# Kernel tuning notes

Hardware: AMD Instinct MI355X
Metric: run time of the kernel (lower is better)

## Reference

```python
import jax, jax.numpy as jnp
import numpy as np
import math

D_K = 64

def setup_inputs() -> dict:
    key = jax.random.key(0)
    kq, kk, kv, km = jax.random.split(key, 4)
    B, H, S, D = 2, 16, 2048, D_K
    Q = jax.random.normal(kq, (B, H, S, D), dtype=jnp.float32)
    K = jax.random.normal(kk, (B, H, S, D), dtype=jnp.float32)
    V = jax.random.normal(kv, (B, H, S, D), dtype=jnp.float32)
    attn_mask = jax.random.randint(km, (B, 1, S, S), 0, 2, dtype=jnp.int32)
    return {"Q": Q, "K": K, "V": V, "attn_mask": attn_mask}

def reference(Q, K, V, attn_mask):
    # scores: [B, H, S, S]
    scores = jnp.einsum('bhqd,bhkd->bhqk', Q, K) / math.sqrt(D_K)
    scores = jnp.where(attn_mask == 0, jnp.float32(-1e9), scores)
    attn = jax.nn.softmax(scores, axis=-1)
    context = jnp.einsum('bhqk,bhkd->bhqd', attn, V)
    return (context, attn)
```

## Files before the change

### kernel.cpp

```cpp
#include <hip/hip_runtime.h>
#include <math.h>

#define B_   2
#define H_   16
#define S_   2048
#define D_   64
#define QT   16
#define NQT  (S_/QT)
#define NBLK (B_*H_*NQT)

typedef __attribute__((ext_vector_type(8))) short  bf16x8;
typedef __attribute__((ext_vector_type(8))) unsigned short u16x8;
typedef __attribute__((ext_vector_type(4))) float  f32x4;

static __device__ __forceinline__ short f2bf(float f) {
    union { float f; unsigned u; } x; x.f = f;
    unsigned r = x.u + 0x7fffu + ((x.u >> 16) & 1u);
    return (short)(r >> 16);
}
static __device__ __forceinline__ unsigned pk_bf16(float lo, float hi) {
    unsigned r;
    asm("v_cvt_pk_bf16_f32 %0, %1, %2" : "=v"(r) : "v"(lo), "v"(hi));
    return r;
}

__global__ __launch_bounds__(256) void cvt_scale_kernel(const float* __restrict__ src,
                                                        unsigned short* __restrict__ dst,
                                                        float scale) {
    const size_t i = ((size_t)blockIdx.x * 256 + threadIdx.x) * 8;
    const float4 a = *(const float4*)(src + i);
    const float4 b = *(const float4*)(src + i + 4);
    u16x8 o;
    o[0]=f2bf(a.x*scale); o[1]=f2bf(a.y*scale); o[2]=f2bf(a.z*scale); o[3]=f2bf(a.w*scale);
    o[4]=f2bf(b.x*scale); o[5]=f2bf(b.y*scale); o[6]=f2bf(b.z*scale); o[7]=f2bf(b.w*scale);
    *(u16x8*)(dst + i) = o;
}

__global__ __launch_bounds__(256) void cvtVT_kernel(const float* __restrict__ V,
                                                    unsigned short* __restrict__ Vt) {
    const int l  = threadIdx.x & 63;
    const int w  = threadIdx.x >> 6;
    const int bh = blockIdx.x >> 6;
    const int kc = (blockIdx.x & 63) * 32 + w * 8;
    const float* vp = V + ((size_t)bh * S_ + kc) * D_ + l;
    u16x8 o;
    #pragma unroll
    for (int j = 0; j < 8; ++j) o[j] = f2bf(vp[(size_t)j * D_]);
    *(u16x8*)(Vt + ((size_t)bh * D_ + l) * S_ + kc) = o;
}

__global__ __launch_bounds__(256) void maskbits_kernel(const int* __restrict__ M,
                                                       unsigned long long* __restrict__ bits) {
    const int w = threadIdx.x >> 6, l = threadIdx.x & 63;
    const size_t wl0 = (size_t)(blockIdx.x * 4 + w) * 32;
    for (int it = 0; it < 32; ++it) {
        const int mk = M[(wl0 + it) * 64 + l];
        const unsigned long long bm = __ballot(mk != 0);
        if (l == 0) bits[wl0 + it] = bm;
    }
}

template<int PREP>
__global__ __launch_bounds__(256, 4)
void sdpa_2pass_kernel(const float* __restrict__ Qf, const float* __restrict__ Kf,
                       const float* __restrict__ Vf, const int* __restrict__ Mi,
                       const unsigned short* __restrict__ Qs,
                       const unsigned short* __restrict__ Kb,
                       const unsigned short* __restrict__ Vt,
                       const unsigned* __restrict__ bits,
                       float* __restrict__ ctx_out, float* __restrict__ attn_out) {
    __shared__ unsigned mb[QT][66];
    __shared__ float red[4][QT][2];
    __shared__ float ctxp[4][QT][68];

    const int t = threadIdx.x;
    const int w = t >> 6;
    const int l = t & 63;
    const int x = l & 15;
    const int g = l >> 4;

    const int orig = blockIdx.x;
    const int swz  = (orig & 7) * (NBLK / 8) + (orig >> 3);
    const int bh   = swz >> 7;
    const int qt   = swz & 127;
    const int b    = bh >> 4;
    const int q0   = qt * QT;

    if (PREP) {
        #pragma unroll
        for (int i = 0; i < 4; ++i) {
            const int flat = t * 4 + i;
            mb[flat >> 6][flat & 63] =
                bits[((size_t)b * S_ + q0 + (flat >> 6)) * 64 + (flat & 63)];
        }
    }

    bf16x8 bq0, bq1;
    if (PREP) {
        const unsigned short* qp = Qs + ((size_t)bh * S_ + q0 + x) * D_ + g * 8;
        bq0 = *(const bf16x8*)qp;
        bq1 = *(const bf16x8*)(qp + 32);
    } else {
        const float* qp = Qf + ((size_t)bh * S_ + q0 + x) * D_ + g * 8;
        #pragma unroll
        for (int j = 0; j < 8; ++j) bq0[j] = f2bf(0.125f * qp[j]);
        #pragma unroll
        for (int j = 0; j < 8; ++j) bq1[j] = f2bf(0.125f * qp[32 + j]);
    }
    if (PREP) __syncthreads();

    auto qk_tile = [&](int ktg, f32x4& c) {
        bf16x8 ak0, ak1;
        if (PREP) {
            const unsigned short* kp = Kb + ((size_t)bh * S_ + ktg * 16 + x) * D_ + g * 8;
            ak0 = *(const bf16x8*)kp;
            ak1 = *(const bf16x8*)(kp + 32);
        } else {
            const float* kp = Kf + ((size_t)bh * S_ + ktg * 16 + x) * D_ + g * 8;
            #pragma unroll
            for (int j = 0; j < 8; ++j) ak0[j] = f2bf(kp[j]);
            #pragma unroll
            for (int j = 0; j < 8; ++j) ak1[j] = f2bf(kp[32 + j]);
        }
        c[0]=0.f; c[1]=0.f; c[2]=0.f; c[3]=0.f;
        c = __builtin_amdgcn_mfma_f32_16x16x32_bf16(ak0, bq0, c, 0, 0, 0);
        c = __builtin_amdgcn_mfma_f32_16x16x32_bf16(ak1, bq1, c, 0, 0, 0);
        if (PREP) {
            const unsigned word = mb[x][ktg >> 1];
            const int base = 16 * (ktg & 1) + 4 * g;
            #pragma unroll
            for (int r = 0; r < 4; ++r)
                if (!((word >> (base + r)) & 1u)) c[r] = -1e9f;
        } else {
            const int* mp = Mi + ((size_t)b * S_ + q0 + x) * S_ + ktg * 16 + 4 * g;
            #pragma unroll
            for (int r = 0; r < 4; ++r)
                if (!mp[r]) c[r] = -1e9f;
        }
    };

    float m = -INFINITY, ssum = 0.f;
    for (int kt = 0; kt < 32; ++kt) {
        f32x4 c; qk_tile(32 * w + kt, c);
        const float tm = fmaxf(fmaxf(c[0], c[1]), fmaxf(c[2], c[3]));
        const float nm = fmaxf(m, tm);
        ssum = ssum * __expf(m - nm)
             + __expf(c[0] - nm) + __expf(c[1] - nm)
             + __expf(c[2] - nm) + __expf(c[3] - nm);
        m = nm;
    }
    #pragma unroll
    for (int off = 16; off <= 32; off <<= 1) {
        const float mo = __shfl_xor(m, off), so = __shfl_xor(ssum, off);
        const float nm = fmaxf(m, mo);
        ssum = ssum * __expf(m - nm) + so * __expf(mo - nm);
        m = nm;
    }
    if (l < 16) { red[w][l][0] = m; red[w][l][1] = ssum; }
    __syncthreads();
    float M = -INFINITY, S = 0.f;
    #pragma unroll
    for (int wv = 0; wv < 4; ++wv) {
        const float mo = red[wv][x][0], so = red[wv][x][1];
        const float nm = fmaxf(M, mo);
        S = S * __expf(M - nm) + so * __expf(mo - nm);
        M = nm;
    }
    const float il = 1.0f / S;

    f32x4 ctx[4];
    #pragma unroll
    for (int ds = 0; ds < 4; ++ds) { ctx[ds][0]=0.f; ctx[ds][1]=0.f; ctx[ds][2]=0.f; ctx[ds][3]=0.f; }

    const int laneA = x + 32 * (g & 1);
    const int laneB = laneA + 16;
    const int tsel  = g >> 1;

    for (int s = 0; s < 16; ++s) {
        unsigned W00, W01, W10, W11;
        #pragma unroll
        for (int u = 0; u < 2; ++u) {
            const int ktg = 32 * w + 2 * s + u;
            f32x4 c; qk_tile(ktg, c);
            const float p0 = __expf(c[0] - M) * il, p1 = __expf(c[1] - M) * il;
            const float p2 = __expf(c[2] - M) * il, p3 = __expf(c[3] - M) * il;
            float4 o; o.x = p0; o.y = p1; o.z = p2; o.w = p3;
            *(float4*)(attn_out + ((size_t)bh * S_ + q0 + x) * S_ + ktg * 16 + 4 * g) = o;
            const unsigned lo = pk_bf16(p0, p1), hi = pk_bf16(p2, p3);
            if (u == 0) { W00 = lo; W01 = hi; } else { W10 = lo; W11 = hi; }
        }
        const unsigned a00 = __shfl(W00, laneA), a10 = __shfl(W10, laneA);
        const unsigned a01 = __shfl(W01, laneA), a11 = __shfl(W11, laneA);
        const unsigned b00 = __shfl(W00, laneB), b10 = __shfl(W10, laneB);
        const unsigned b01 = __shfl(W01, laneB), b11 = __shfl(W11, laneB);
        union { unsigned u[4]; bf16x8 v; } pa;
        pa.u[0] = tsel ? a10 : a00;
        pa.u[1] = tsel ? a11 : a01;
        pa.u[2] = tsel ? b10 : b00;
        pa.u[3] = tsel ? b11 : b01;
        const int kb = 512 * w + 32 * s;
        #pragma unroll
        for (int ds = 0; ds < 4; ++ds) {
            bf16x8 vb;
            if (PREP) {
                vb = *(const bf16x8*)(Vt + ((size_t)bh * D_ + 16 * ds + x) * S_ + kb + 8 * g);
            } else {
                const float* vp = Vf + ((size_t)bh * S_ + kb + 8 * g) * D_ + 16 * ds + x;
                #pragma unroll
                for (int j = 0; j < 8; ++j) vb[j] = f2bf(vp[(size_t)j * D_]);
            }
            ctx[ds] = __builtin_amdgcn_mfma_f32_16x16x32_bf16(pa.v, vb, ctx[ds], 0, 0, 0);
        }
    }

    #pragma unroll
    for (int ds = 0; ds < 4; ++ds)
        #pragma unroll
        for (int r = 0; r < 4; ++r)
            ctxp[w][4 * g + r][16 * ds + x] = ctx[ds][r];
    __syncthreads();
    {
        const int base = t * 4;
        const int qr = base >> 6, c0 = base & 63;
        float4 o;
        o.x = ctxp[0][qr][c0+0] + ctxp[1][qr][c0+0] + ctxp[2][qr][c0+0] + ctxp[3][qr][c0+0];
        o.y = ctxp[0][qr][c0+1] + ctxp[1][qr][c0+1] + ctxp[2][qr][c0+1] + ctxp[3][qr][c0+1];
        o.z = ctxp[0][qr][c0+2] + ctxp[1][qr][c0+2] + ctxp[2][qr][c0+2] + ctxp[3][qr][c0+2];
        o.w = ctxp[0][qr][c0+3] + ctxp[1][qr][c0+3] + ctxp[2][qr][c0+3] + ctxp[3][qr][c0+3];
        *(float4*)(ctx_out + ((size_t)bh * S_ + q0 + qr) * D_ + c0) = o;
    }
}

extern "C" void kernel_launch(void* const* d_in, const int* in_sizes, int n_in,
                              void* d_out, int out_size, void* d_ws, size_t ws_size,
                              hipStream_t stream) {
    const float* Q = (const float*)d_in[0];
    const float* K = (const float*)d_in[1];
    const float* V = (const float*)d_in[2];
    const int*   M = (const int*)d_in[3];

    float* ctx  = (float*)d_out;
    float* attn = (float*)d_out + (size_t)B_ * H_ * S_ * D_;

    const size_t nEl     = (size_t)B_ * H_ * S_ * D_;
    const size_t nBits64 = (size_t)B_ * S_ * (S_ / 64);
    const size_t need    = nEl * 2 * 3 + nBits64 * 8;

    if (ws_size >= need) {
        unsigned short* Qs = (unsigned short*)d_ws;
        unsigned short* Kb = Qs + nEl;
        unsigned short* Vt = Kb + nEl;
        unsigned long long* bits = (unsigned long long*)(Vt + nEl);
        cvt_scale_kernel<<<dim3((int)(nEl / 2048)), dim3(256), 0, stream>>>(Q, Qs, 0.125f);
        cvt_scale_kernel<<<dim3((int)(nEl / 2048)), dim3(256), 0, stream>>>(K, Kb, 1.0f);
        cvtVT_kernel    <<<dim3(B_ * H_ * (S_ / 32)), dim3(256), 0, stream>>>(V, Vt);
        maskbits_kernel <<<dim3((int)(nBits64 / 128)), dim3(256), 0, stream>>>(M, bits);
        sdpa_2pass_kernel<1><<<dim3(NBLK), dim3(256), 0, stream>>>(
            Q, K, V, M, Qs, Kb, Vt, (const unsigned*)bits, ctx, attn);
    } else {
        sdpa_2pass_kernel<0><<<dim3(NBLK), dim3(256), 0, stream>>>(
            Q, K, V, M, nullptr, nullptr, nullptr, nullptr, ctx, attn);
    }
}
```

Measured before the change: 426.6 us.

## Cache QK scores in registers as bf16 instead of recomputing in second pass

```diff
diff --git a/kernel.cpp b/kernel.cpp
--- a/kernel.cpp
+++ b/kernel.cpp
@@ -22,6 +22,12 @@
     unsigned r;
     asm("v_cvt_pk_bf16_f32 %0, %1, %2" : "=v"(r) : "v"(lo), "v"(hi));
     return r;
+}
+static __device__ __forceinline__ float bfLo(unsigned w) {
+    union { unsigned u; float f; } x; x.u = w << 16; return x.f;
+}
+static __device__ __forceinline__ float bfHi(unsigned w) {
+    union { unsigned u; float f; } x; x.u = w & 0xffff0000u; return x.f;
 }
 
 __global__ __launch_bounds__(256) void cvt_scale_kernel(const float* __restrict__ src,
@@ -62,13 +68,13 @@
 
 template<int PREP>
 __global__ __launch_bounds__(256, 4)
-void sdpa_2pass_kernel(const float* __restrict__ Qf, const float* __restrict__ Kf,
-                       const float* __restrict__ Vf, const int* __restrict__ Mi,
-                       const unsigned short* __restrict__ Qs,
-                       const unsigned short* __restrict__ Kb,
-                       const unsigned short* __restrict__ Vt,
-                       const unsigned* __restrict__ bits,
-                       float* __restrict__ ctx_out, float* __restrict__ attn_out) {
+void sdpa_1qk_kernel(const float* __restrict__ Qf, const float* __restrict__ Kf,
+                     const float* __restrict__ Vf, const int* __restrict__ Mi,
+                     const unsigned short* __restrict__ Qs,
+                     const unsigned short* __restrict__ Kb,
+                     const unsigned short* __restrict__ Vt,
+                     const unsigned* __restrict__ bits,
+                     float* __restrict__ ctx_out, float* __restrict__ attn_out) {
     __shared__ unsigned mb[QT][66];
     __shared__ float red[4][QT][2];
     __shared__ float ctxp[4][QT][68];
@@ -109,7 +115,11 @@
     }
     if (PREP) __syncthreads();
 
-    auto qk_tile = [&](int ktg, f32x4& c) {
+    unsigned sp[64];
+    float m = -INFINITY, ssum = 0.f;
+    #pragma unroll
+    for (int kt = 0; kt < 32; ++kt) {
+        const int ktg = 32 * w + kt;
         bf16x8 ak0, ak1;
         if (PREP) {
             const unsigned short* kp = Kb + ((size_t)bh * S_ + ktg * 16 + x) * D_ + g * 8;
@@ -122,7 +132,7 @@
             #pragma unroll
             for (int j = 0; j < 8; ++j) ak1[j] = f2bf(kp[32 + j]);
         }
-        c[0]=0.f; c[1]=0.f; c[2]=0.f; c[3]=0.f;
+        f32x4 c = {0.f, 0.f, 0.f, 0.f};
         c = __builtin_amdgcn_mfma_f32_16x16x32_bf16(ak0, bq0, c, 0, 0, 0);
         c = __builtin_amdgcn_mfma_f32_16x16x32_bf16(ak1, bq1, c, 0, 0, 0);
         if (PREP) {
@@ -137,11 +147,8 @@
             for (int r = 0; r < 4; ++r)
                 if (!mp[r]) c[r] = -1e9f;
         }
-    };
-
-    float m = -INFINITY, ssum = 0.f;
-    for (int kt = 0; kt < 32; ++kt) {
-        f32x4 c; qk_tile(32 * w + kt, c);
+        sp[2 * kt]     = pk_bf16(c[0], c[1]);
+        sp[2 * kt + 1] = pk_bf16(c[2], c[3]);
         const float tm = fmaxf(fmaxf(c[0], c[1]), fmaxf(c[2], c[3]));
         const float nm = fmaxf(m, tm);
         ssum = ssum * __expf(m - nm)
@@ -176,16 +183,15 @@
     const int laneB = laneA + 16;
     const int tsel  = g >> 1;
 
+    #pragma unroll
     for (int s = 0; s < 16; ++s) {
         unsigned W00, W01, W10, W11;
         #pragma unroll
         for (int u = 0; u < 2; ++u) {
-            const int ktg = 32 * w + 2 * s + u;
-            f32x4 c; qk_tile(ktg, c);
-            const float p0 = __expf(c[0] - M) * il, p1 = __expf(c[1] - M) * il;
-            const float p2 = __expf(c[2] - M) * il, p3 = __expf(c[3] - M) * il;
-            float4 o; o.x = p0; o.y = p1; o.z = p2; o.w = p3;
-            *(float4*)(attn_out + ((size_t)bh * S_ + q0 + x) * S_ + ktg * 16 + 4 * g) = o;
+            const unsigned wa = sp[4 * s + 2 * u];
+            const unsigned wb = sp[4 * s + 2 * u + 1];
+            const float p0 = __expf(bfLo(wa) - M) * il, p1 = __expf(bfHi(wa) - M) * il;
+            const float p2 = __expf(bfLo(wb) - M) * il, p3 = __expf(bfHi(wb) - M) * il;
             const unsigned lo = pk_bf16(p0, p1), hi = pk_bf16(p2, p3);
             if (u == 0) { W00 = lo; W01 = hi; } else { W10 = lo; W11 = hi; }
         }
@@ -210,6 +216,20 @@
                 for (int j = 0; j < 8; ++j) vb[j] = f2bf(vp[(size_t)j * D_]);
             }
             ctx[ds] = __builtin_amdgcn_mfma_f32_16x16x32_bf16(pa.v, vb, ctx[ds], 0, 0, 0);
+        }
+    }
+
+    {
+        float* arow = attn_out + ((size_t)bh * S_ + q0 + x) * S_ + 512 * w + 4 * g;
+        #pragma unroll
+        for (int kt = 0; kt < 32; ++kt) {
+            const unsigned wa = sp[2 * kt], wb = sp[2 * kt + 1];
+            float4 o;
+            o.x = __expf(bfLo(wa) - M) * il;
+            o.y = __expf(bfHi(wa) - M) * il;
+            o.z = __expf(bfLo(wb) - M) * il;
+            o.w = __expf(bfHi(wb) - M) * il;
+            *(float4*)(arow + kt * 16) = o;
         }
     }
 
@@ -255,10 +275,10 @@
         cvt_scale_kernel<<<dim3((int)(nEl / 2048)), dim3(256), 0, stream>>>(K, Kb, 1.0f);
         cvtVT_kernel    <<<dim3(B_ * H_ * (S_ / 32)), dim3(256), 0, stream>>>(V, Vt);
         maskbits_kernel <<<dim3((int)(nBits64 / 128)), dim3(256), 0, stream>>>(M, bits);
-        sdpa_2pass_kernel<1><<<dim3(NBLK), dim3(256), 0, stream>>>(
+        sdpa_1qk_kernel<1><<<dim3(NBLK), dim3(256), 0, stream>>>(
             Q, K, V, M, Qs, Kb, Vt, (const unsigned*)bits, ctx, attn);
     } else {
-        sdpa_2pass_kernel<0><<<dim3(NBLK), dim3(256), 0, stream>>>(
+        sdpa_1qk_kernel<0><<<dim3(NBLK), dim3(256), 0, stream>>>(
             Q, K, V, M, nullptr, nullptr, nullptr, nullptr, ctx, attn);
     }
 }
```

After: 407.0 us. 1.05x faster.
